# Kernel optimization log

Measured on AMD Instinct MI355X. Metric: run time of the kernel, lower is better.

Reference implementation:

```python
import jax, jax.numpy as jnp
import numpy as np

N = 1024
IN_F = 128
H0 = 192  # num_features * 2
H1 = 96   # num_features * 1
BN_EPS = 1e-5
SLOPE = 0.01  # LeakyReLU default negative slope


def setup_inputs() -> dict:
    key = jax.random.key(0)
    ks = jax.random.split(key, 8)
    node_feat = jax.random.normal(ks[0], (N, IN_F), dtype=jnp.float32)
    W0 = jax.random.normal(ks[1], (H0, IN_F), dtype=jnp.float32) * 0.05
    g0 = jnp.ones((H0,), jnp.float32); b0 = jnp.zeros((H0,), jnp.float32)
    m0 = jnp.zeros((H0,), jnp.float32); v0 = jnp.ones((H0,), jnp.float32)
    W1 = jax.random.normal(ks[2], (H1, H0), dtype=jnp.float32) * 0.05
    g1 = jnp.ones((H1,), jnp.float32); b1 = jnp.zeros((H1,), jnp.float32)
    m1 = jnp.zeros((H1,), jnp.float32); v1 = jnp.ones((H1,), jnp.float32)
    Wout = jax.random.normal(ks[3], (1, H1), dtype=jnp.float32) * 0.05
    bout = jnp.zeros((1,), jnp.float32)
    return dict(node_feat=node_feat, W0=W0, g0=g0, b0=b0, m0=m0, v0=v0,
                W1=W1, g1=g1, b1=b1, m1=m1, v1=v1, Wout=Wout, bout=bout)


def _bn(x, g, b, m, v):
    # BatchNorm2d in eval mode over channel axis (last axis here)
    return (x - m) * (g * jax.lax.rsqrt(v + BN_EPS)) + b


def _leaky(x):
    return jnp.where(x >= 0, x, SLOPE * x)


def reference(node_feat, W0, g0, b0, m0, v0, W1, g1, b1, m1, v1, Wout, bout):
    n = node_feat.shape[0]
    # pairwise abs diff: [N, N, F] (symmetric, so torch's i/j transpose is a no-op)
    x_ij = jnp.abs(node_feat[:, None, :] - node_feat[None, :, :])
    # 1x1 convs == per-(i,j) matmuls over channel axis
    h = _leaky(_bn(jnp.einsum('ijf,cf->ijc', x_ij, W0), g0, b0, m0, v0))
    h = _leaky(_bn(jnp.einsum('ijc,dc->ijd', h, W1), g1, b1, m1, v1))
    logits = jnp.einsum('ijd,od->ijo', h, Wout)[..., 0] + bout[0]  # [N, N]
    sim_val = jax.nn.sigmoid(logits)
    edge = sim_val + jnp.eye(n, dtype=sim_val.dtype) + 1e-6
    # torch sums over dim=1 of [1, N, N] -> normalize over the row index i
    edge = edge / jnp.sum(edge, axis=0, keepdims=True)
    return edge[None], sim_val  # edge_feat [1, N, N], sim_val [N, N]
```

## Files before the change

kernel.cpp:

```cpp
#include <hip/hip_runtime.h>
#include <hip/hip_bf16.h>
#include <math.h>

typedef float v4f __attribute__((ext_vector_type(4)));
typedef __bf16 bf16x8 __attribute__((ext_vector_type(8)));

#define NN   1024
#define INF  128
#define H0C  192
#define H1C  96

#define WS_W0BF   0
#define WS_W1BF   49152
#define WS_BN0B   86016
#define WS_BN1B   86784
#define WS_WOUT   87168
#define WS_CINV   87552
#define WS_PART   91648

__global__ __launch_bounds__(256) void prep_kernel(
    const float* __restrict__ W0, const float* __restrict__ g0,
    const float* __restrict__ b0, const float* __restrict__ m0,
    const float* __restrict__ v0, const float* __restrict__ W1,
    const float* __restrict__ g1, const float* __restrict__ b1,
    const float* __restrict__ m1, const float* __restrict__ v1,
    const float* __restrict__ Wout, char* __restrict__ ws)
{
    int e = blockIdx.x * 256 + threadIdx.x;
    __bf16* w0bf = (__bf16*)(ws + WS_W0BF);
    __bf16* w1bf = (__bf16*)(ws + WS_W1BF);
    float* bn0b = (float*)(ws + WS_BN0B);
    float* bn1b = (float*)(ws + WS_BN1B);
    float* wout = (float*)(ws + WS_WOUT);
    if (e < 24576) {
        int j = e & 7, lane = (e >> 3) & 63, t = e >> 9;
        int ks = t & 3, nt = t >> 2;
        int c = nt * 16 + (lane & 15);
        int k = ks * 32 + ((lane >> 4) << 3) + j;
        float s = g0[c] * rsqrtf(v0[c] + 1e-5f);
        w0bf[e] = (__bf16)(W0[c * INF + k] * s);
    } else if (e < 43008) {
        int e2 = e - 24576;
        int j = e2 & 7, lane = (e2 >> 3) & 63, t = e2 >> 9;
        int ks = t % 6, nt = t / 6;
        int c = nt * 16 + (lane & 15);
        int k = ks * 32 + ((lane >> 4) << 3) + j;
        float s = g1[c] * rsqrtf(v1[c] + 1e-5f);
        w1bf[e2] = (__bf16)(W1[c * H0C + k] * s);
    } else if (e < 43200) {
        int c = e - 43008;
        float s = g0[c] * rsqrtf(v0[c] + 1e-5f);
        bn0b[c] = b0[c] - m0[c] * s;
    } else if (e < 43296) {
        int c = e - 43200;
        float s = g1[c] * rsqrtf(v1[c] + 1e-5f);
        bn1b[c] = b1[c] - m1[c] * s;
    } else if (e < 43392) {
        int c = e - 43296;
        wout[c] = Wout[c];
    }
}

__global__ __launch_bounds__(256, 2) void edgenet_main(
    const float* __restrict__ feat, const char* __restrict__ ws,
    const float* __restrict__ boutp, float* __restrict__ sim_out)
{
    __shared__ __align__(16) char smem[51200];
    const int tid = threadIdx.x;
    const int lane = tid & 63;
    const int wave = tid >> 6;
    const int l16 = lane & 15;
    const int quad = lane >> 4;

    const int id = blockIdx.x;
    int bi = (int)((129.0f - sqrtf(16641.0f - 4.0f * (float)id)) * 0.5f);
    while (bi * (129 - bi) > id) --bi;
    while ((bi + 1) * (128 - bi) <= id) ++bi;
    const int bj = 2 * bi + (id - bi * (129 - bi));
    const int i0 = bi << 4;
    const int j0 = bj << 3;

    #pragma unroll
    for (int it = 0; it < 8; ++it) {
        int c = it * 256 + tid;
        int p = c >> 4;
        int f0 = (c & 15) << 3;
        int ii = p & 15, jj = p >> 4;
        const float* fi = feat + (i0 + ii) * INF + f0;
        const float* fj = feat + (j0 + jj) * INF + f0;
        float4 a0 = *(const float4*)fi;
        float4 a1 = *(const float4*)(fi + 4);
        float4 q0 = *(const float4*)fj;
        float4 q1 = *(const float4*)(fj + 4);
        bf16x8 x;
        x[0] = (__bf16)fabsf(a0.x - q0.x);
        x[1] = (__bf16)fabsf(a0.y - q0.y);
        x[2] = (__bf16)fabsf(a0.z - q0.z);
        x[3] = (__bf16)fabsf(a0.w - q0.w);
        x[4] = (__bf16)fabsf(a1.x - q1.x);
        x[5] = (__bf16)fabsf(a1.y - q1.y);
        x[6] = (__bf16)fabsf(a1.z - q1.z);
        x[7] = (__bf16)fabsf(a1.w - q1.w);
        *(bf16x8*)(smem + p * 272 + f0 * 2) = x;
    }
    __syncthreads();

    const int mbase = wave << 5;
    bf16x8 afrag[2][4];
    #pragma unroll
    for (int mt = 0; mt < 2; ++mt)
        #pragma unroll
        for (int ks = 0; ks < 4; ++ks)
            afrag[mt][ks] = *(const bf16x8*)(smem +
                (mbase + mt * 16 + l16) * 272 + ks * 64 + quad * 16);
    __syncthreads();

    const bf16x8* w0v = (const bf16x8*)(ws + WS_W0BF);
    const float* bn0b = (const float*)(ws + WS_BN0B);
    v4f acc1[2][12];
    #pragma unroll
    for (int nt = 0; nt < 12; ++nt) {
        float bb = bn0b[nt * 16 + l16];
        acc1[0][nt] = (v4f){bb, bb, bb, bb};
        acc1[1][nt] = acc1[0][nt];
    }
    #pragma unroll
    for (int nt = 0; nt < 12; ++nt) {
        #pragma unroll
        for (int ks = 0; ks < 4; ++ks) {
            bf16x8 b = w0v[(nt * 4 + ks) * 64 + lane];
            acc1[0][nt] = __builtin_amdgcn_mfma_f32_16x16x32_bf16(
                afrag[0][ks], b, acc1[0][nt], 0, 0, 0);
            acc1[1][nt] = __builtin_amdgcn_mfma_f32_16x16x32_bf16(
                afrag[1][ks], b, acc1[1][nt], 0, 0, 0);
        }
    }

    #pragma unroll
    for (int nt = 0; nt < 12; ++nt) {
        int cch = nt * 16 + l16;
        #pragma unroll
        for (int mt = 0; mt < 2; ++mt)
            #pragma unroll
            for (int r = 0; r < 4; ++r) {
                float v = acc1[mt][nt][r];
                v = fmaxf(v, 0.01f * v);
                int m = mbase + mt * 16 + quad * 4 + r;
                *(__bf16*)(smem + m * 400 + cch * 2) = (__bf16)v;
            }
    }
    __syncthreads();

    bf16x8 a2[2][6];
    #pragma unroll
    for (int mt = 0; mt < 2; ++mt)
        #pragma unroll
        for (int ks = 0; ks < 6; ++ks)
            a2[mt][ks] = *(const bf16x8*)(smem +
                (mbase + mt * 16 + l16) * 400 + ks * 64 + quad * 16);

    const bf16x8* w1v = (const bf16x8*)(ws + WS_W1BF);
    const float* bn1b = (const float*)(ws + WS_BN1B);
    v4f acc2[2][6];
    #pragma unroll
    for (int nt = 0; nt < 6; ++nt) {
        float bb = bn1b[nt * 16 + l16];
        acc2[0][nt] = (v4f){bb, bb, bb, bb};
        acc2[1][nt] = acc2[0][nt];
    }
    #pragma unroll
    for (int nt = 0; nt < 6; ++nt) {
        #pragma unroll
        for (int ks = 0; ks < 6; ++ks) {
            bf16x8 b = w1v[(nt * 6 + ks) * 64 + lane];
            acc2[0][nt] = __builtin_amdgcn_mfma_f32_16x16x32_bf16(
                a2[0][ks], b, acc2[0][nt], 0, 0, 0);
            acc2[1][nt] = __builtin_amdgcn_mfma_f32_16x16x32_bf16(
                a2[1][ks], b, acc2[1][nt], 0, 0, 0);
        }
    }

    const float* wout = (const float*)(ws + WS_WOUT);
    float part[2][4] = {{0.f, 0.f, 0.f, 0.f}, {0.f, 0.f, 0.f, 0.f}};
    #pragma unroll
    for (int nt = 0; nt < 6; ++nt) {
        float wo = wout[nt * 16 + l16];
        #pragma unroll
        for (int mt = 0; mt < 2; ++mt)
            #pragma unroll
            for (int r = 0; r < 4; ++r) {
                float v = acc2[mt][nt][r];
                v = fmaxf(v, 0.01f * v);
                part[mt][r] = fmaf(v, wo, part[mt][r]);
            }
    }
    #pragma unroll
    for (int off = 1; off < 16; off <<= 1) {
        #pragma unroll
        for (int mt = 0; mt < 2; ++mt)
            #pragma unroll
            for (int r = 0; r < 4; ++r)
                part[mt][r] += __shfl_xor(part[mt][r], off, 64);
    }
    if (l16 == 0) {
        float bout0 = boutp[0];
        #pragma unroll
        for (int mt = 0; mt < 2; ++mt)
            #pragma unroll
            for (int r = 0; r < 4; ++r) {
                int m = mbase + mt * 16 + quad * 4 + r;
                int ii = m & 15, jj = m >> 4;
                float logit = part[mt][r] + bout0;
                float sv = 1.f / (1.f + expf(-logit));
                sim_out[(i0 + ii) * NN + (j0 + jj)] = sv;
                sim_out[(j0 + jj) * NN + (i0 + ii)] = sv;
            }
    }
}

__global__ __launch_bounds__(256) void colsum_kernel(
    const float* __restrict__ sim, float* __restrict__ part)
{
    __shared__ float red[4][64];
    int jl = threadIdx.x & 63;
    int ig = threadIdx.x >> 6;
    int j = blockIdx.x * 64 + jl;
    int ibase = blockIdx.y * 64 + ig * 16;
    float s = 0.f;
    #pragma unroll
    for (int r = 0; r < 16; ++r)
        s += sim[(ibase + r) * NN + j];
    red[ig][jl] = s;
    __syncthreads();
    if (ig == 0) {
        float t = red[0][jl] + red[1][jl] + red[2][jl] + red[3][jl];
        part[blockIdx.y * NN + j] = t;
    }
}

__global__ __launch_bounds__(256) void finalize_kernel(
    const float* __restrict__ part, float* __restrict__ cinv)
{
    int j = blockIdx.x * 256 + threadIdx.x;
    float s = 0.f;
    #pragma unroll
    for (int p = 0; p < 16; ++p)
        s += part[p * NN + j];
    cinv[j] = 1.0f / (s + 1.0f + (float)NN * 1e-6f);
}

__global__ __launch_bounds__(256) void edge_kernel(
    const float* __restrict__ sim, const float* __restrict__ cinv,
    float* __restrict__ edge)
{
    int gid = blockIdx.x * 256 + threadIdx.x;
    int i = gid >> 8;
    int jc = (gid & 255) << 2;
    float4 s = *(const float4*)(sim + i * NN + jc);
    float4 w = *(const float4*)(cinv + jc);
    float4 o;
    o.x = (s.x + (i == jc + 0 ? 1.f : 0.f) + 1e-6f) * w.x;
    o.y = (s.y + (i == jc + 1 ? 1.f : 0.f) + 1e-6f) * w.y;
    o.z = (s.z + (i == jc + 2 ? 1.f : 0.f) + 1e-6f) * w.z;
    o.w = (s.w + (i == jc + 3 ? 1.f : 0.f) + 1e-6f) * w.w;
    *(float4*)(edge + i * NN + jc) = o;
}

extern "C" void kernel_launch(void* const* d_in, const int* in_sizes, int n_in,
                              void* d_out, int out_size, void* d_ws, size_t ws_size,
                              hipStream_t stream)
{
    const float* feat = (const float*)d_in[0];
    const float* W0   = (const float*)d_in[1];
    const float* g0   = (const float*)d_in[2];
    const float* b0   = (const float*)d_in[3];
    const float* m0   = (const float*)d_in[4];
    const float* v0   = (const float*)d_in[5];
    const float* W1   = (const float*)d_in[6];
    const float* g1   = (const float*)d_in[7];
    const float* b1   = (const float*)d_in[8];
    const float* m1   = (const float*)d_in[9];
    const float* v1   = (const float*)d_in[10];
    const float* Wout = (const float*)d_in[11];
    const float* bout = (const float*)d_in[12];
    char* ws = (char*)d_ws;
    float* edge = (float*)d_out;
    float* sim  = edge + NN * NN;
    float* cinv = (float*)(ws + WS_CINV);
    float* part = (float*)(ws + WS_PART);

    prep_kernel<<<dim3(170), dim3(256), 0, stream>>>(
        W0, g0, b0, m0, v0, W1, g1, b1, m1, v1, Wout, ws);
    edgenet_main<<<dim3(4160), dim3(256), 0, stream>>>(feat, ws, bout, sim);
    colsum_kernel<<<dim3(16, 16), dim3(256), 0, stream>>>(sim, part);
    finalize_kernel<<<dim3(4), dim3(256), 0, stream>>>(part, cinv);
    edge_kernel<<<dim3(1024), dim3(256), 0, stream>>>(sim, cinv, edge);
}
```

Before: 162.5 us.

## Keep MLP intermediates in registers via transposed MFMA chaining, drop shared memory

The main kernel now computes the transposed product (weights as the A operand, pair differences as B), so the first layer's accumulator layout directly feeds the second layer's 16x16x16 bf16 MFMA as a B fragment. This removes all shared-memory staging, the block barriers and the LDS round trip between layers. The prep kernel reorders W1, the BN biases and Wout into matching swizzled layouts. Blocks now cover 16x16 upper-triangle tiles, halving the grid. Register pressure rises, and the smaller 16x16x16 MFMA shape has lower throughput per instruction.

```diff
diff --git a/kernel.cpp b/kernel.cpp
--- a/kernel.cpp
+++ b/kernel.cpp
@@ -4,6 +4,8 @@
 
 typedef float v4f __attribute__((ext_vector_type(4)));
 typedef __bf16 bf16x8 __attribute__((ext_vector_type(8)));
+typedef __bf16 bf16x4 __attribute__((ext_vector_type(4)));
+typedef short  s4v   __attribute__((ext_vector_type(4)));
 
 #define NN   1024
 #define INF  128
@@ -12,11 +14,13 @@
 
 #define WS_W0BF   0
 #define WS_W1BF   49152
-#define WS_BN0B   86016
-#define WS_BN1B   86784
-#define WS_WOUT   87168
+#define WS_BN0SW  86016
+#define WS_BN1SW  86784
+#define WS_WOUTSW 87168
 #define WS_CINV   87552
 #define WS_PART   91648
+
+union bf4cast { bf16x4 b; s4v s; };
 
 __global__ __launch_bounds__(256) void prep_kernel(
     const float* __restrict__ W0, const float* __restrict__ g0,
@@ -29,35 +33,40 @@
     int e = blockIdx.x * 256 + threadIdx.x;
     __bf16* w0bf = (__bf16*)(ws + WS_W0BF);
     __bf16* w1bf = (__bf16*)(ws + WS_W1BF);
-    float* bn0b = (float*)(ws + WS_BN0B);
-    float* bn1b = (float*)(ws + WS_BN1B);
-    float* wout = (float*)(ws + WS_WOUT);
+    float* bn0sw = (float*)(ws + WS_BN0SW);
+    float* bn1sw = (float*)(ws + WS_BN1SW);
+    float* woutsw = (float*)(ws + WS_WOUTSW);
     if (e < 24576) {
         int j = e & 7, lane = (e >> 3) & 63, t = e >> 9;
-        int ks = t & 3, nt = t >> 2;
-        int c = nt * 16 + (lane & 15);
+        int ks = t & 3, ct = t >> 2;
+        int c = ct * 16 + (lane & 15);
         int k = ks * 32 + ((lane >> 4) << 3) + j;
         float s = g0[c] * rsqrtf(v0[c] + 1e-5f);
         w0bf[e] = (__bf16)(W0[c * INF + k] * s);
     } else if (e < 43008) {
         int e2 = e - 24576;
-        int j = e2 & 7, lane = (e2 >> 3) & 63, t = e2 >> 9;
-        int ks = t % 6, nt = t / 6;
-        int c = nt * 16 + (lane & 15);
-        int k = ks * 32 + ((lane >> 4) << 3) + j;
-        float s = g1[c] * rsqrtf(v1[c] + 1e-5f);
-        w1bf[e2] = (__bf16)(W1[c * H0C + k] * s);
+        int j = e2 & 3, lane = (e2 >> 2) & 63, t = e2 >> 8;
+        int ct = t % 12, dt = t / 12;
+        int d = dt * 16 + (lane & 15);
+        int c = ct * 16 + ((lane >> 4) << 2) + j;
+        float s = g1[d] * rsqrtf(v1[d] + 1e-5f);
+        w1bf[e2] = (__bf16)(W1[d * H0C + c] * s);
     } else if (e < 43200) {
-        int c = e - 43008;
+        int e3 = e - 43008;
+        int q = e3 / 48, rem = e3 % 48, ct = rem >> 2, r = rem & 3;
+        int c = ct * 16 + q * 4 + r;
         float s = g0[c] * rsqrtf(v0[c] + 1e-5f);
-        bn0b[c] = b0[c] - m0[c] * s;
+        bn0sw[e3] = b0[c] - m0[c] * s;
     } else if (e < 43296) {
-        int c = e - 43200;
-        float s = g1[c] * rsqrtf(v1[c] + 1e-5f);
-        bn1b[c] = b1[c] - m1[c] * s;
+        int e4 = e - 43200;
+        int q = e4 / 24, rem = e4 % 24, dt = rem >> 2, r = rem & 3;
+        int d = dt * 16 + q * 4 + r;
+        float s = g1[d] * rsqrtf(v1[d] + 1e-5f);
+        bn1sw[e4] = b1[d] - m1[d] * s;
     } else if (e < 43392) {
-        int c = e - 43296;
-        wout[c] = Wout[c];
+        int e5 = e - 43296;
+        int q = e5 / 24, rem = e5 % 24, dt = rem >> 2, r = rem & 3;
+        woutsw[e5] = Wout[dt * 16 + q * 4 + r];
     }
 }
 
@@ -65,7 +74,6 @@
     const float* __restrict__ feat, const char* __restrict__ ws,
     const float* __restrict__ boutp, float* __restrict__ sim_out)
 {
-    __shared__ __align__(16) char smem[51200];
     const int tid = threadIdx.x;
     const int lane = tid & 63;
     const int wave = tid >> 6;
@@ -73,149 +81,121 @@
     const int quad = lane >> 4;
 
     const int id = blockIdx.x;
-    int bi = (int)((129.0f - sqrtf(16641.0f - 4.0f * (float)id)) * 0.5f);
-    while (bi * (129 - bi) > id) --bi;
-    while ((bi + 1) * (128 - bi) <= id) ++bi;
-    const int bj = 2 * bi + (id - bi * (129 - bi));
+    int bi = (int)((129.0f - sqrtf(16641.0f - 8.0f * (float)id)) * 0.5f);
+    if (bi > 63) bi = 63;
+    while (bi > 0 && bi * (129 - bi) / 2 > id) --bi;
+    while ((bi + 1) * (128 - bi) / 2 <= id) ++bi;
+    const int bj = bi + (id - bi * (129 - bi) / 2);
     const int i0 = bi << 4;
-    const int j0 = bj << 3;
-
-    #pragma unroll
-    for (int it = 0; it < 8; ++it) {
-        int c = it * 256 + tid;
-        int p = c >> 4;
-        int f0 = (c & 15) << 3;
-        int ii = p & 15, jj = p >> 4;
-        const float* fi = feat + (i0 + ii) * INF + f0;
-        const float* fj = feat + (j0 + jj) * INF + f0;
+    const int j0 = bj << 4;
+    const int jjb = j0 + wave * 4;
+
+    bf16x8 xf[4][4];
+    #pragma unroll
+    for (int ks = 0; ks < 4; ++ks) {
+        const float* fi = feat + (i0 + l16) * INF + ks * 32 + quad * 8;
         float4 a0 = *(const float4*)fi;
         float4 a1 = *(const float4*)(fi + 4);
-        float4 q0 = *(const float4*)fj;
-        float4 q1 = *(const float4*)(fj + 4);
-        bf16x8 x;
-        x[0] = (__bf16)fabsf(a0.x - q0.x);
-        x[1] = (__bf16)fabsf(a0.y - q0.y);
-        x[2] = (__bf16)fabsf(a0.z - q0.z);
-        x[3] = (__bf16)fabsf(a0.w - q0.w);
-        x[4] = (__bf16)fabsf(a1.x - q1.x);
-        x[5] = (__bf16)fabsf(a1.y - q1.y);
-        x[6] = (__bf16)fabsf(a1.z - q1.z);
-        x[7] = (__bf16)fabsf(a1.w - q1.w);
-        *(bf16x8*)(smem + p * 272 + f0 * 2) = x;
-    }
-    __syncthreads();
-
-    const int mbase = wave << 5;
-    bf16x8 afrag[2][4];
-    #pragma unroll
-    for (int mt = 0; mt < 2; ++mt)
-        #pragma unroll
-        for (int ks = 0; ks < 4; ++ks)
-            afrag[mt][ks] = *(const bf16x8*)(smem +
-                (mbase + mt * 16 + l16) * 272 + ks * 64 + quad * 16);
-    __syncthreads();
+        #pragma unroll
+        for (int nt = 0; nt < 4; ++nt) {
+            const float* fj = feat + (jjb + nt) * INF + ks * 32 + quad * 8;
+            float4 q0 = *(const float4*)fj;
+            float4 q1 = *(const float4*)(fj + 4);
+            bf16x8 x;
+            x[0] = (__bf16)fabsf(a0.x - q0.x);
+            x[1] = (__bf16)fabsf(a0.y - q0.y);
+            x[2] = (__bf16)fabsf(a0.z - q0.z);
+            x[3] = (__bf16)fabsf(a0.w - q0.w);
+            x[4] = (__bf16)fabsf(a1.x - q1.x);
+            x[5] = (__bf16)fabsf(a1.y - q1.y);
+            x[6] = (__bf16)fabsf(a1.z - q1.z);
+            x[7] = (__bf16)fabsf(a1.w - q1.w);
+            xf[ks][nt] = x;
+        }
+    }
+
+    const float* bn1sw = (const float*)(ws + WS_BN1SW);
+    v4f acc2[4][6];
+    #pragma unroll
+    for (int dt = 0; dt < 6; ++dt) {
+        v4f bb = *(const v4f*)(bn1sw + (quad * 6 + dt) * 4);
+        #pragma unroll
+        for (int nt = 0; nt < 4; ++nt)
+            acc2[nt][dt] = bb;
+    }
 
     const bf16x8* w0v = (const bf16x8*)(ws + WS_W0BF);
-    const float* bn0b = (const float*)(ws + WS_BN0B);
-    v4f acc1[2][12];
-    #pragma unroll
-    for (int nt = 0; nt < 12; ++nt) {
-        float bb = bn0b[nt * 16 + l16];
-        acc1[0][nt] = (v4f){bb, bb, bb, bb};
-        acc1[1][nt] = acc1[0][nt];
-    }
-    #pragma unroll
-    for (int nt = 0; nt < 12; ++nt) {
-        #pragma unroll
-        for (int ks = 0; ks < 4; ++ks) {
-            bf16x8 b = w0v[(nt * 4 + ks) * 64 + lane];
-            acc1[0][nt] = __builtin_amdgcn_mfma_f32_16x16x32_bf16(
-                afrag[0][ks], b, acc1[0][nt], 0, 0, 0);
-            acc1[1][nt] = __builtin_amdgcn_mfma_f32_16x16x32_bf16(
-                afrag[1][ks], b, acc1[1][nt], 0, 0, 0);
-        }
-    }
-
-    #pragma unroll
-    for (int nt = 0; nt < 12; ++nt) {
-        int cch = nt * 16 + l16;
-        #pragma unroll
-        for (int mt = 0; mt < 2; ++mt)
+    const __bf16* w1p = (const __bf16*)(ws + WS_W1BF);
+    const float* bn0sw = (const float*)(ws + WS_BN0SW);
+    #pragma unroll
+    for (int ct = 0; ct < 12; ++ct) {
+        v4f b0v = *(const v4f*)(bn0sw + (quad * 12 + ct) * 4);
+        v4f a1[4];
+        {
+            bf16x8 w = w0v[(ct * 4 + 0) * 64 + lane];
+            #pragma unroll
+            for (int nt = 0; nt < 4; ++nt)
+                a1[nt] = __builtin_amdgcn_mfma_f32_16x16x32_bf16(
+                    w, xf[0][nt], b0v, 0, 0, 0);
+        }
+        #pragma unroll
+        for (int ks = 1; ks < 4; ++ks) {
+            bf16x8 w = w0v[(ct * 4 + ks) * 64 + lane];
+            #pragma unroll
+            for (int nt = 0; nt < 4; ++nt)
+                a1[nt] = __builtin_amdgcn_mfma_f32_16x16x32_bf16(
+                    w, xf[ks][nt], a1[nt], 0, 0, 0);
+        }
+        s4v b2[4];
+        #pragma unroll
+        for (int nt = 0; nt < 4; ++nt) {
+            bf4cast u;
             #pragma unroll
             for (int r = 0; r < 4; ++r) {
-                float v = acc1[mt][nt][r];
+                float v = a1[nt][r];
                 v = fmaxf(v, 0.01f * v);
-                int m = mbase + mt * 16 + quad * 4 + r;
-                *(__bf16*)(smem + m * 400 + cch * 2) = (__bf16)v;
+                u.b[r] = (__bf16)v;
             }
-    }
-    __syncthreads();
-
-    bf16x8 a2[2][6];
-    #pragma unroll
-    for (int mt = 0; mt < 2; ++mt)
-        #pragma unroll
-        for (int ks = 0; ks < 6; ++ks)
-            a2[mt][ks] = *(const bf16x8*)(smem +
-                (mbase + mt * 16 + l16) * 400 + ks * 64 + quad * 16);
-
-    const bf16x8* w1v = (const bf16x8*)(ws + WS_W1BF);
-    const float* bn1b = (const float*)(ws + WS_BN1B);
-    v4f acc2[2][6];
-    #pragma unroll
-    for (int nt = 0; nt < 6; ++nt) {
-        float bb = bn1b[nt * 16 + l16];
-        acc2[0][nt] = (v4f){bb, bb, bb, bb};
-        acc2[1][nt] = acc2[0][nt];
-    }
-    #pragma unroll
-    for (int nt = 0; nt < 6; ++nt) {
-        #pragma unroll
-        for (int ks = 0; ks < 6; ++ks) {
-            bf16x8 b = w1v[(nt * 6 + ks) * 64 + lane];
-            acc2[0][nt] = __builtin_amdgcn_mfma_f32_16x16x32_bf16(
-                a2[0][ks], b, acc2[0][nt], 0, 0, 0);
-            acc2[1][nt] = __builtin_amdgcn_mfma_f32_16x16x32_bf16(
-                a2[1][ks], b, acc2[1][nt], 0, 0, 0);
-        }
-    }
-
-    const float* wout = (const float*)(ws + WS_WOUT);
-    float part[2][4] = {{0.f, 0.f, 0.f, 0.f}, {0.f, 0.f, 0.f, 0.f}};
-    #pragma unroll
-    for (int nt = 0; nt < 6; ++nt) {
-        float wo = wout[nt * 16 + l16];
-        #pragma unroll
-        for (int mt = 0; mt < 2; ++mt)
+            b2[nt] = u.s;
+        }
+        #pragma unroll
+        for (int dt = 0; dt < 6; ++dt) {
+            s4v w1f = *(const s4v*)(w1p + ((dt * 12 + ct) * 64 + lane) * 4);
+            #pragma unroll
+            for (int nt = 0; nt < 4; ++nt)
+                acc2[nt][dt] = __builtin_amdgcn_mfma_f32_16x16x16bf16_1k(
+                    w1f, b2[nt], acc2[nt][dt], 0, 0, 0);
+        }
+    }
+
+    const float* woutsw = (const float*)(ws + WS_WOUTSW);
+    float part[4] = {0.f, 0.f, 0.f, 0.f};
+    #pragma unroll
+    for (int dt = 0; dt < 6; ++dt) {
+        v4f wo = *(const v4f*)(woutsw + (quad * 6 + dt) * 4);
+        #pragma unroll
+        for (int nt = 0; nt < 4; ++nt) {
             #pragma unroll
             for (int r = 0; r < 4; ++r) {
-                float v = acc2[mt][nt][r];
+                float v = acc2[nt][dt][r];
                 v = fmaxf(v, 0.01f * v);
-                part[mt][r] = fmaf(v, wo, part[mt][r]);
+                part[nt] = fmaf(v, wo[r], part[nt]);
             }
-    }
-    #pragma unroll
-    for (int off = 1; off < 16; off <<= 1) {
-        #pragma unroll
-        for (int mt = 0; mt < 2; ++mt)
-            #pragma unroll
-            for (int r = 0; r < 4; ++r)
-                part[mt][r] += __shfl_xor(part[mt][r], off, 64);
-    }
-    if (l16 == 0) {
-        float bout0 = boutp[0];
-        #pragma unroll
-        for (int mt = 0; mt < 2; ++mt)
-            #pragma unroll
-            for (int r = 0; r < 4; ++r) {
-                int m = mbase + mt * 16 + quad * 4 + r;
-                int ii = m & 15, jj = m >> 4;
-                float logit = part[mt][r] + bout0;
-                float sv = 1.f / (1.f + expf(-logit));
-                sim_out[(i0 + ii) * NN + (j0 + jj)] = sv;
-                sim_out[(j0 + jj) * NN + (i0 + ii)] = sv;
-            }
-    }
+        }
+    }
+    #pragma unroll
+    for (int nt = 0; nt < 4; ++nt) {
+        part[nt] += __shfl_xor(part[nt], 16, 64);
+        part[nt] += __shfl_xor(part[nt], 32, 64);
+    }
+    float sel = quad < 2 ? (quad == 0 ? part[0] : part[1])
+                         : (quad == 2 ? part[2] : part[3]);
+    float logit = sel + boutp[0];
+    float sv = 1.f / (1.f + expf(-logit));
+    const int irow = i0 + l16;
+    const int jcol = jjb + quad;
+    sim_out[irow * NN + jcol] = sv;
+    sim_out[jcol * NN + irow] = sv;
 }
 
 __global__ __launch_bounds__(256) void colsum_kernel(
@@ -291,7 +271,7 @@
 
     prep_kernel<<<dim3(170), dim3(256), 0, stream>>>(
         W0, g0, b0, m0, v0, W1, g1, b1, m1, v1, Wout, ws);
-    edgenet_main<<<dim3(4160), dim3(256), 0, stream>>>(feat, ws, bout, sim);
+    edgenet_main<<<dim3(2080), dim3(256), 0, stream>>>(feat, ws, bout, sim);
     colsum_kernel<<<dim3(16, 16), dim3(256), 0, stream>>>(sim, part);
     finalize_kernel<<<dim3(4), dim3(256), 0, stream>>>(part, cinv);
     edge_kernel<<<dim3(1024), dim3(256), 0, stream>>>(sim, cinv, edge);
```

New measurement: 201.3 us. +23.9%, slower.

## Fuse column-sum into main kernel via atomics and split layer-0 into halves

Applied to the files above, without the earlier changes.

Drops the separate colsum and finalize kernels. Column sums are now accumulated with atomics inside the main kernel, using a zeroed buffer set up in prep. Each wave builds its pairwise abs-diff fragments directly in registers instead of staging them in shared memory. Layer 0 is computed in two 96-channel halves that feed layer 1 incrementally, which shrinks shared memory and register pressure so the launch bound can rise to 3 blocks per CU. The costs are atomic contention on the column sums, nondeterministic summation order, and __syncthreads inside the half loop.

```diff
diff --git a/kernel.cpp b/kernel.cpp
--- a/kernel.cpp
+++ b/kernel.cpp
@@ -15,8 +15,7 @@
 #define WS_BN0B   86016
 #define WS_BN1B   86784
 #define WS_WOUT   87168
-#define WS_CINV   87552
-#define WS_PART   91648
+#define WS_CSUM   87552
 
 __global__ __launch_bounds__(256) void prep_kernel(
     const float* __restrict__ W0, const float* __restrict__ g0,
@@ -32,6 +31,7 @@
     float* bn0b = (float*)(ws + WS_BN0B);
     float* bn1b = (float*)(ws + WS_BN1B);
     float* wout = (float*)(ws + WS_WOUT);
+    float* csum = (float*)(ws + WS_CSUM);
     if (e < 24576) {
         int j = e & 7, lane = (e >> 3) & 63, t = e >> 9;
         int ks = t & 3, nt = t >> 2;
@@ -56,16 +56,18 @@
         float s = g1[c] * rsqrtf(v1[c] + 1e-5f);
         bn1b[c] = b1[c] - m1[c] * s;
     } else if (e < 43392) {
-        int c = e - 43296;
-        wout[c] = Wout[c];
-    }
-}
-
-__global__ __launch_bounds__(256, 2) void edgenet_main(
+        wout[e - 43296] = Wout[e - 43296];
+    } else if (e < 44416) {
+        csum[e - 43392] = 0.f;
+    }
+}
+
+__global__ __launch_bounds__(256, 3) void edgenet_main(
     const float* __restrict__ feat, const char* __restrict__ ws,
-    const float* __restrict__ boutp, float* __restrict__ sim_out)
-{
-    __shared__ __align__(16) char smem[51200];
+    const float* __restrict__ boutp, float* __restrict__ sim_out,
+    float* __restrict__ colsum)
+{
+    __shared__ __align__(16) char smem[26624];
     const int tid = threadIdx.x;
     const int lane = tid & 63;
     const int wave = tid >> 6;
@@ -74,195 +76,166 @@
 
     const int id = blockIdx.x;
     int bi = (int)((129.0f - sqrtf(16641.0f - 4.0f * (float)id)) * 0.5f);
-    while (bi * (129 - bi) > id) --bi;
+    while (bi > 0 && bi * (129 - bi) > id) --bi;
     while ((bi + 1) * (128 - bi) <= id) ++bi;
     const int bj = 2 * bi + (id - bi * (129 - bi));
     const int i0 = bi << 4;
-    const int j0 = bj << 3;
-
-    #pragma unroll
-    for (int it = 0; it < 8; ++it) {
-        int c = it * 256 + tid;
-        int p = c >> 4;
-        int f0 = (c & 15) << 3;
-        int ii = p & 15, jj = p >> 4;
-        const float* fi = feat + (i0 + ii) * INF + f0;
-        const float* fj = feat + (j0 + jj) * INF + f0;
+    const int jb = (bj << 3) + wave * 2;
+    char* hbase = smem + wave * 6656;
+
+    bf16x8 xf[2][4];
+    #pragma unroll
+    for (int ks = 0; ks < 4; ++ks) {
+        const float* fi = feat + (i0 + l16) * INF + ks * 32 + quad * 8;
         float4 a0 = *(const float4*)fi;
         float4 a1 = *(const float4*)(fi + 4);
-        float4 q0 = *(const float4*)fj;
-        float4 q1 = *(const float4*)(fj + 4);
-        bf16x8 x;
-        x[0] = (__bf16)fabsf(a0.x - q0.x);
-        x[1] = (__bf16)fabsf(a0.y - q0.y);
-        x[2] = (__bf16)fabsf(a0.z - q0.z);
-        x[3] = (__bf16)fabsf(a0.w - q0.w);
-        x[4] = (__bf16)fabsf(a1.x - q1.x);
-        x[5] = (__bf16)fabsf(a1.y - q1.y);
-        x[6] = (__bf16)fabsf(a1.z - q1.z);
-        x[7] = (__bf16)fabsf(a1.w - q1.w);
-        *(bf16x8*)(smem + p * 272 + f0 * 2) = x;
-    }
-    __syncthreads();
-
-    const int mbase = wave << 5;
-    bf16x8 afrag[2][4];
-    #pragma unroll
-    for (int mt = 0; mt < 2; ++mt)
-        #pragma unroll
-        for (int ks = 0; ks < 4; ++ks)
-            afrag[mt][ks] = *(const bf16x8*)(smem +
-                (mbase + mt * 16 + l16) * 272 + ks * 64 + quad * 16);
-    __syncthreads();
+        #pragma unroll
+        for (int mt = 0; mt < 2; ++mt) {
+            const float* fj = feat + (jb + mt) * INF + ks * 32 + quad * 8;
+            float4 q0 = *(const float4*)fj;
+            float4 q1 = *(const float4*)(fj + 4);
+            bf16x8 x;
+            x[0] = (__bf16)fabsf(a0.x - q0.x);
+            x[1] = (__bf16)fabsf(a0.y - q0.y);
+            x[2] = (__bf16)fabsf(a0.z - q0.z);
+            x[3] = (__bf16)fabsf(a0.w - q0.w);
+            x[4] = (__bf16)fabsf(a1.x - q1.x);
+            x[5] = (__bf16)fabsf(a1.y - q1.y);
+            x[6] = (__bf16)fabsf(a1.z - q1.z);
+            x[7] = (__bf16)fabsf(a1.w - q1.w);
+            xf[mt][ks] = x;
+        }
+    }
 
     const bf16x8* w0v = (const bf16x8*)(ws + WS_W0BF);
+    const bf16x8* w1v = (const bf16x8*)(ws + WS_W1BF);
     const float* bn0b = (const float*)(ws + WS_BN0B);
-    v4f acc1[2][12];
-    #pragma unroll
-    for (int nt = 0; nt < 12; ++nt) {
-        float bb = bn0b[nt * 16 + l16];
-        acc1[0][nt] = (v4f){bb, bb, bb, bb};
-        acc1[1][nt] = acc1[0][nt];
-    }
-    #pragma unroll
-    for (int nt = 0; nt < 12; ++nt) {
-        #pragma unroll
-        for (int ks = 0; ks < 4; ++ks) {
-            bf16x8 b = w0v[(nt * 4 + ks) * 64 + lane];
-            acc1[0][nt] = __builtin_amdgcn_mfma_f32_16x16x32_bf16(
-                afrag[0][ks], b, acc1[0][nt], 0, 0, 0);
-            acc1[1][nt] = __builtin_amdgcn_mfma_f32_16x16x32_bf16(
-                afrag[1][ks], b, acc1[1][nt], 0, 0, 0);
-        }
-    }
-
-    #pragma unroll
-    for (int nt = 0; nt < 12; ++nt) {
-        int cch = nt * 16 + l16;
+    const float* bn1b = (const float*)(ws + WS_BN1B);
+
+    v4f acc2[2][6];
+    #pragma unroll
+    for (int nt2 = 0; nt2 < 6; ++nt2) {
+        float bb = bn1b[nt2 * 16 + l16];
+        acc2[0][nt2] = (v4f){bb, bb, bb, bb};
+        acc2[1][nt2] = acc2[0][nt2];
+    }
+
+    #pragma unroll 1
+    for (int h = 0; h < 2; ++h) {
+        v4f acc1[2][6];
+        #pragma unroll
+        for (int nt = 0; nt < 6; ++nt) {
+            float bb = bn0b[h * 96 + nt * 16 + l16];
+            v4f c0 = (v4f){bb, bb, bb, bb};
+            bf16x8 w = w0v[((h * 6 + nt) * 4 + 0) * 64 + lane];
+            acc1[0][nt] = __builtin_amdgcn_mfma_f32_16x16x32_bf16(xf[0][0], w, c0, 0, 0, 0);
+            acc1[1][nt] = __builtin_amdgcn_mfma_f32_16x16x32_bf16(xf[1][0], w, c0, 0, 0, 0);
+            #pragma unroll
+            for (int ks = 1; ks < 4; ++ks) {
+                bf16x8 w2 = w0v[((h * 6 + nt) * 4 + ks) * 64 + lane];
+                acc1[0][nt] = __builtin_amdgcn_mfma_f32_16x16x32_bf16(xf[0][ks], w2, acc1[0][nt], 0, 0, 0);
+                acc1[1][nt] = __builtin_amdgcn_mfma_f32_16x16x32_bf16(xf[1][ks], w2, acc1[1][nt], 0, 0, 0);
+            }
+        }
+        #pragma unroll
+        for (int nt = 0; nt < 6; ++nt) {
+            int col = nt * 16 + l16;
+            #pragma unroll
+            for (int mt = 0; mt < 2; ++mt)
+                #pragma unroll
+                for (int r = 0; r < 4; ++r) {
+                    float v = acc1[mt][nt][r];
+                    v = fmaxf(v, 0.01f * v);
+                    int row = mt * 16 + quad * 4 + r;
+                    *(__bf16*)(hbase + row * 208 + col * 2) = (__bf16)v;
+                }
+        }
+        bf16x8 a2[2][3];
         #pragma unroll
         for (int mt = 0; mt < 2; ++mt)
             #pragma unroll
-            for (int r = 0; r < 4; ++r) {
-                float v = acc1[mt][nt][r];
-                v = fmaxf(v, 0.01f * v);
-                int m = mbase + mt * 16 + quad * 4 + r;
-                *(__bf16*)(smem + m * 400 + cch * 2) = (__bf16)v;
-            }
-    }
-    __syncthreads();
-
-    bf16x8 a2[2][6];
-    #pragma unroll
-    for (int mt = 0; mt < 2; ++mt)
-        #pragma unroll
-        for (int ks = 0; ks < 6; ++ks)
-            a2[mt][ks] = *(const bf16x8*)(smem +
-                (mbase + mt * 16 + l16) * 400 + ks * 64 + quad * 16);
-
-    const bf16x8* w1v = (const bf16x8*)(ws + WS_W1BF);
-    const float* bn1b = (const float*)(ws + WS_BN1B);
-    v4f acc2[2][6];
-    #pragma unroll
-    for (int nt = 0; nt < 6; ++nt) {
-        float bb = bn1b[nt * 16 + l16];
-        acc2[0][nt] = (v4f){bb, bb, bb, bb};
-        acc2[1][nt] = acc2[0][nt];
-    }
-    #pragma unroll
-    for (int nt = 0; nt < 6; ++nt) {
-        #pragma unroll
-        for (int ks = 0; ks < 6; ++ks) {
-            bf16x8 b = w1v[(nt * 6 + ks) * 64 + lane];
-            acc2[0][nt] = __builtin_amdgcn_mfma_f32_16x16x32_bf16(
-                a2[0][ks], b, acc2[0][nt], 0, 0, 0);
-            acc2[1][nt] = __builtin_amdgcn_mfma_f32_16x16x32_bf16(
-                a2[1][ks], b, acc2[1][nt], 0, 0, 0);
-        }
+            for (int ks2 = 0; ks2 < 3; ++ks2)
+                a2[mt][ks2] = *(const bf16x8*)(hbase +
+                    (mt * 16 + l16) * 208 + ks2 * 64 + quad * 16);
+        #pragma unroll
+        for (int nt2 = 0; nt2 < 6; ++nt2) {
+            #pragma unroll
+            for (int ks2 = 0; ks2 < 3; ++ks2) {
+                bf16x8 w = w1v[(nt2 * 6 + h * 3 + ks2) * 64 + lane];
+                acc2[0][nt2] = __builtin_amdgcn_mfma_f32_16x16x32_bf16(a2[0][ks2], w, acc2[0][nt2], 0, 0, 0);
+                acc2[1][nt2] = __builtin_amdgcn_mfma_f32_16x16x32_bf16(a2[1][ks2], w, acc2[1][nt2], 0, 0, 0);
+            }
+        }
+        __syncthreads();
     }
 
     const float* wout = (const float*)(ws + WS_WOUT);
     float part[2][4] = {{0.f, 0.f, 0.f, 0.f}, {0.f, 0.f, 0.f, 0.f}};
     #pragma unroll
-    for (int nt = 0; nt < 6; ++nt) {
-        float wo = wout[nt * 16 + l16];
+    for (int nt2 = 0; nt2 < 6; ++nt2) {
+        float wo = wout[nt2 * 16 + l16];
         #pragma unroll
         for (int mt = 0; mt < 2; ++mt)
             #pragma unroll
             for (int r = 0; r < 4; ++r) {
-                float v = acc2[mt][nt][r];
+                float v = acc2[mt][nt2][r];
                 v = fmaxf(v, 0.01f * v);
                 part[mt][r] = fmaf(v, wo, part[mt][r]);
             }
     }
     #pragma unroll
-    for (int off = 1; off < 16; off <<= 1) {
+    for (int off = 1; off < 16; off <<= 1)
         #pragma unroll
         for (int mt = 0; mt < 2; ++mt)
             #pragma unroll
             for (int r = 0; r < 4; ++r)
                 part[mt][r] += __shfl_xor(part[mt][r], off, 64);
+    float b0s = boutp[0];
+    float sv[2][4];
+    #pragma unroll
+    for (int mt = 0; mt < 2; ++mt)
+        #pragma unroll
+        for (int r = 0; r < 4; ++r)
+            sv[mt][r] = 1.f / (1.f + expf(-(part[mt][r] + b0s)));
+
+    #pragma unroll
+    for (int mt = 0; mt < 2; ++mt) {
+        float t = sv[mt][0] + sv[mt][1] + sv[mt][2] + sv[mt][3];
+        t += __shfl_xor(t, 16, 64);
+        t += __shfl_xor(t, 32, 64);
+        if (lane == 0) atomicAdd(colsum + jb + mt, t);
     }
     if (l16 == 0) {
-        float bout0 = boutp[0];
-        #pragma unroll
-        for (int mt = 0; mt < 2; ++mt)
+        #pragma unroll
+        for (int mt = 0; mt < 2; ++mt) {
+            int jcol = jb + mt;
+            float4 m4 = {sv[mt][0], sv[mt][1], sv[mt][2], sv[mt][3]};
+            *(float4*)(sim_out + jcol * NN + i0 + quad * 4) = m4;
             #pragma unroll
             for (int r = 0; r < 4; ++r) {
-                int m = mbase + mt * 16 + quad * 4 + r;
-                int ii = m & 15, jj = m >> 4;
-                float logit = part[mt][r] + bout0;
-                float sv = 1.f / (1.f + expf(-logit));
-                sim_out[(i0 + ii) * NN + (j0 + jj)] = sv;
-                sim_out[(j0 + jj) * NN + (i0 + ii)] = sv;
-            }
-    }
-}
-
-__global__ __launch_bounds__(256) void colsum_kernel(
-    const float* __restrict__ sim, float* __restrict__ part)
-{
-    __shared__ float red[4][64];
-    int jl = threadIdx.x & 63;
-    int ig = threadIdx.x >> 6;
-    int j = blockIdx.x * 64 + jl;
-    int ibase = blockIdx.y * 64 + ig * 16;
-    float s = 0.f;
-    #pragma unroll
-    for (int r = 0; r < 16; ++r)
-        s += sim[(ibase + r) * NN + j];
-    red[ig][jl] = s;
-    __syncthreads();
-    if (ig == 0) {
-        float t = red[0][jl] + red[1][jl] + red[2][jl] + red[3][jl];
-        part[blockIdx.y * NN + j] = t;
-    }
-}
-
-__global__ __launch_bounds__(256) void finalize_kernel(
-    const float* __restrict__ part, float* __restrict__ cinv)
-{
-    int j = blockIdx.x * 256 + threadIdx.x;
-    float s = 0.f;
-    #pragma unroll
-    for (int p = 0; p < 16; ++p)
-        s += part[p * NN + j];
-    cinv[j] = 1.0f / (s + 1.0f + (float)NN * 1e-6f);
+                int irow = i0 + quad * 4 + r;
+                sim_out[irow * NN + jcol] = sv[mt][r];
+                if (!((irow >> 3) >= 2 * (jcol >> 4)))
+                    atomicAdd(colsum + irow, sv[mt][r]);
+            }
+        }
+    }
 }
 
 __global__ __launch_bounds__(256) void edge_kernel(
-    const float* __restrict__ sim, const float* __restrict__ cinv,
+    const float* __restrict__ colsum, const float* __restrict__ sim,
     float* __restrict__ edge)
 {
-    int gid = blockIdx.x * 256 + threadIdx.x;
-    int i = gid >> 8;
-    int jc = (gid & 255) << 2;
+    int i = blockIdx.x;
+    int jc = threadIdx.x << 2;
+    float4 cs = *(const float4*)(colsum + jc);
+    const float cadd = 1.0f + (float)NN * 1e-6f;
     float4 s = *(const float4*)(sim + i * NN + jc);
-    float4 w = *(const float4*)(cinv + jc);
     float4 o;
-    o.x = (s.x + (i == jc + 0 ? 1.f : 0.f) + 1e-6f) * w.x;
-    o.y = (s.y + (i == jc + 1 ? 1.f : 0.f) + 1e-6f) * w.y;
-    o.z = (s.z + (i == jc + 2 ? 1.f : 0.f) + 1e-6f) * w.z;
-    o.w = (s.w + (i == jc + 3 ? 1.f : 0.f) + 1e-6f) * w.w;
+    o.x = (s.x + (i == jc + 0 ? 1.f : 0.f) + 1e-6f) / (cs.x + cadd);
+    o.y = (s.y + (i == jc + 1 ? 1.f : 0.f) + 1e-6f) / (cs.y + cadd);
+    o.z = (s.z + (i == jc + 2 ? 1.f : 0.f) + 1e-6f) / (cs.z + cadd);
+    o.w = (s.w + (i == jc + 3 ? 1.f : 0.f) + 1e-6f) / (cs.w + cadd);
     *(float4*)(edge + i * NN + jc) = o;
 }
 
@@ -286,13 +259,10 @@
     char* ws = (char*)d_ws;
     float* edge = (float*)d_out;
     float* sim  = edge + NN * NN;
-    float* cinv = (float*)(ws + WS_CINV);
-    float* part = (float*)(ws + WS_PART);
-
-    prep_kernel<<<dim3(170), dim3(256), 0, stream>>>(
+    float* csum = (float*)(ws + WS_CSUM);
+
+    prep_kernel<<<dim3(174), dim3(256), 0, stream>>>(
         W0, g0, b0, m0, v0, W1, g1, b1, m1, v1, Wout, ws);
-    edgenet_main<<<dim3(4160), dim3(256), 0, stream>>>(feat, ws, bout, sim);
-    colsum_kernel<<<dim3(16, 16), dim3(256), 0, stream>>>(sim, part);
-    finalize_kernel<<<dim3(4), dim3(256), 0, stream>>>(part, cinv);
-    edge_kernel<<<dim3(1024), dim3(256), 0, stream>>>(sim, cinv, edge);
-}
+    edgenet_main<<<dim3(4160), dim3(256), 0, stream>>>(feat, ws, bout, sim, csum);
+    edge_kernel<<<dim3(1024), dim3(256), 0, stream>>>(csum, sim, edge);
+}
```

Measured after the change: 328.2 us. +102.0%, slower.
